# Performance work log

Measured on AMD Instinct MI355X. Metric: run time of the kernel, lower is better.

The kernel has to match this reference:

```python
import jax, jax.numpy as jnp
import numpy as np

NODES_PER_GRAPH = 116
HEADS = 2
D_HEAD = 116  # out_channels per head
HID = 256
B = 512
N = B * NODES_PER_GRAPH
DEG = 8
E = N * DEG
D_OUT = HEADS * D_HEAD  # 232


def setup_inputs() -> dict:
    key = jax.random.key(0)
    ks = jax.random.split(key, 6)
    h_flat = jax.random.normal(ks[0], (N, HID), dtype=jnp.float32)
    # every node receives DEG edges from random nodes within its own 116-node graph
    dst = jnp.repeat(jnp.arange(N, dtype=jnp.int64), DEG)
    offs = jax.random.randint(ks[1], (E,), 0, NODES_PER_GRAPH, dtype=jnp.int64)
    src = (dst // NODES_PER_GRAPH) * NODES_PER_GRAPH + offs
    edge_index = jnp.stack([src, dst], axis=0)
    batch_index = jnp.repeat(jnp.arange(B, dtype=jnp.int64), NODES_PER_GRAPH)
    s = 1.0 / np.sqrt(HID)
    Wq = jax.random.normal(ks[2], (HID, D_OUT), dtype=jnp.float32) * s
    Wk = jax.random.normal(ks[3], (HID, D_OUT), dtype=jnp.float32) * s
    Wv = jax.random.normal(ks[4], (HID, D_OUT), dtype=jnp.float32) * s
    Ws = jax.random.normal(ks[5], (HID, D_OUT), dtype=jnp.float32) * s
    return {"h_flat": h_flat, "edge_index": edge_index, "batch_index": batch_index,
            "Wq": Wq, "Wk": Wk, "Wv": Wv, "Ws": Ws}


def _graph_transformer_layer(h, edge_index, Wq, Wk, Wv, Ws):
    # PyG TransformerConv-style multi-head edge attention, concat heads + root skip.
    n = h.shape[0]
    q = (h @ Wq).reshape(n, HEADS, D_HEAD)
    k = (h @ Wk).reshape(n, HEADS, D_HEAD)
    v = (h @ Wv).reshape(n, HEADS, D_HEAD)
    src, dst = edge_index[0], edge_index[1]
    # per-edge scores [E, H]
    scores = jnp.einsum('ehd,ehd->eh', q[dst], k[src]) / np.sqrt(D_HEAD)
    # segment softmax over incoming edges of each dst node
    m = jax.ops.segment_max(scores, dst, num_segments=n)
    m = jnp.where(jnp.isfinite(m), m, 0.0)
    ex = jnp.exp(scores - m[dst])
    denom = jax.ops.segment_sum(ex, dst, num_segments=n)
    alpha_e = ex / (denom[dst] + 1e-16)
    msg = alpha_e[:, :, None] * v[src]                      # [E, H, Dh]
    attn = jax.ops.segment_sum(msg, dst, num_segments=n)    # [N, H, Dh]
    return attn.reshape(n, D_OUT) + h @ Ws


def reference(h_flat, edge_index, batch_index, Wq, Wk, Wv, Ws):
    n = h_flat.shape[0]
    b = n // NODES_PER_GRAPH
    h_proj = _graph_transformer_layer(h_flat, edge_index, Wq, Wk, Wv, Ws)  # [N, 232]
    e = h_proj.mean(axis=-1)                                 # [N]
    # scatter_softmax over per-graph node segments
    em = jax.ops.segment_max(e, batch_index, num_segments=b)
    ee = jnp.exp(e - em[batch_index])
    es = jax.ops.segment_sum(ee, batch_index, num_segments=b)
    alpha = ee / es[batch_index]                             # [N]
    h_weighted = alpha[:, None] * h_proj                     # [N, 232]
    alpha_map = alpha.reshape(b, NODES_PER_GRAPH)            # [B, 116]
    return alpha_map, h_weighted
```

## Files before the change

kernel.cpp:

```cpp
#include <hip/hip_runtime.h>

#define NODES  116
#define HEADS  2
#define DH     116
#define HID    256
#define NGRAPH 512
#define NN     (NGRAPH*NODES)
#define DEG    8
#define DOUT   (HEADS*DH)
#define NCOLS  928
#define NB_N   8
#define MB_N   464

typedef short  s8v  __attribute__((ext_vector_type(8)));
typedef float  f4v  __attribute__((ext_vector_type(4)));

static __device__ __forceinline__ float bf2f(unsigned short u) {
    union { unsigned int i; float f; } c; c.i = ((unsigned int)u) << 16; return c.f;
}
static __device__ __forceinline__ unsigned short f2bf(float f) {
    union { float f; unsigned int u; } c; c.f = f;
    unsigned int u = c.u;
    unsigned int r = (u + 0x7FFFu + ((u >> 16) & 1u)) >> 16;
    return (unsigned short)r;
}

#define GLD_LDS16(gptr, lptr) \
    __builtin_amdgcn_global_load_lds((const __attribute__((address_space(1))) void*)(gptr), \
                                     (__attribute__((address_space(3))) void*)(lptr), 16, 0, 0)

__global__ __launch_bounds__(256) void prep_h(const float* __restrict__ h,
                                              unsigned short* __restrict__ hs)
{
    unsigned int f = blockIdx.x * 256 + threadIdx.x;
    unsigned int m    = f & 127;
    unsigned int quad = (f >> 7) & 3;
    unsigned int kb   = (f >> 9) & 7;
    unsigned int Mb   = f >> 12;
    unsigned int row  = Mb * 128 + m;
    unsigned int k    = kb * 32 + quad * 8;
    const float4 v0 = *(const float4*)(h + (size_t)row * HID + k);
    const float4 v1 = *(const float4*)(h + (size_t)row * HID + k + 4);
    unsigned short o[8] = { f2bf(v0.x), f2bf(v0.y), f2bf(v0.z), f2bf(v0.w),
                            f2bf(v1.x), f2bf(v1.y), f2bf(v1.z), f2bf(v1.w) };
    *(uint4*)(hs + (size_t)f * 8) = *(const uint4*)o;
}

__global__ __launch_bounds__(256) void prep_w(const float* __restrict__ Wq,
                                              const float* __restrict__ Wk,
                                              const float* __restrict__ Wv,
                                              const float* __restrict__ Ws,
                                              unsigned short* __restrict__ wt)
{
    unsigned int f = blockIdx.x * 256 + threadIdx.x;
    unsigned int n    = f & 127;
    unsigned int quad = (f >> 7) & 3;
    unsigned int kb   = (f >> 9) & 7;
    unsigned int Nb   = f >> 12;
    unsigned int gcol = Nb * 128 + n;
    unsigned int k    = kb * 32 + quad * 8;
    unsigned short o[8] = {0,0,0,0,0,0,0,0};
    if (gcol < NCOLS) {
        unsigned int sel = gcol / DOUT;
        unsigned int col = gcol - sel * DOUT;
        const float* W = (sel == 0) ? Wq : (sel == 1) ? Wk : (sel == 2) ? Wv : Ws;
        #pragma unroll
        for (int i = 0; i < 8; i++)
            o[i] = f2bf(W[(size_t)(k + i) * DOUT + col]);
    }
    *(uint4*)(wt + (size_t)f * 8) = *(const uint4*)o;
}

__global__ __launch_bounds__(256) void gemm_mfma(const unsigned short* __restrict__ hs,
                                                 const unsigned short* __restrict__ wt,
                                                 unsigned short* __restrict__ qkvs)
{
    __shared__ unsigned short lds[17408];
    unsigned short* aA = lds;
    unsigned short* bB = lds + 4096;

    const int by  = blockIdx.x;
    const int bx  = blockIdx.y;
    const int tid = threadIdx.x;
    const int w    = tid >> 6;
    const int lane = tid & 63;
    const int wr   = w >> 1;
    const int wc   = w & 1;
    const int l15  = lane & 15;
    const int quad = lane >> 4;

    f4v acc[4][4];
    #pragma unroll
    for (int mt = 0; mt < 4; mt++)
        #pragma unroll
        for (int nt = 0; nt < 4; nt++)
            #pragma unroll
            for (int r = 0; r < 4; r++) acc[mt][nt][r] = 0.0f;

    for (int kb = 0; kb < 8; kb++) {
        const char* gA = (const char*)(hs + ((size_t)(bx * 8 + kb)) * 4096);
        const char* gB = (const char*)(wt + ((size_t)(by * 8 + kb)) * 4096);
        #pragma unroll
        for (int j = 0; j < 2; j++) {
            int c = w * 2 + j;
            GLD_LDS16(gA + (c * 64 + lane) * 16, (char*)aA + c * 1024);
            GLD_LDS16(gB + (c * 64 + lane) * 16, (char*)bB + c * 1024);
        }
        __syncthreads();

        s8v a[4], b[4];
        #pragma unroll
        for (int mt = 0; mt < 4; mt++) {
            int m = wr * 64 + mt * 16 + l15;
            a[mt] = *(const s8v*)(aA + (quad * 128 + m) * 8);
        }
        #pragma unroll
        for (int nt = 0; nt < 4; nt++) {
            int n = wc * 64 + nt * 16 + l15;
            b[nt] = *(const s8v*)(bB + (quad * 128 + n) * 8);
        }
        #pragma unroll
        for (int mt = 0; mt < 4; mt++)
            #pragma unroll
            for (int nt = 0; nt < 4; nt++)
                acc[mt][nt] = __builtin_amdgcn_mfma_f32_16x16x32_bf16(
                    a[mt], b[nt], acc[mt][nt], 0, 0, 0);
        __syncthreads();
    }

    unsigned short* cb = lds;
    #pragma unroll
    for (int mt = 0; mt < 4; mt++) {
        #pragma unroll
        for (int nt = 0; nt < 4; nt++) {
            int col = wc * 64 + nt * 16 + l15;
            #pragma unroll
            for (int r = 0; r < 4; r++) {
                int row = wr * 64 + mt * 16 + quad * 4 + r;
                cb[row * 136 + col] = f2bf(acc[mt][nt][r]);
            }
        }
    }
    __syncthreads();

    #pragma unroll
    for (int i = 0; i < 8; i++) {
        int g   = tid + i * 256;
        int row = g >> 4;
        int gi  = g & 15;
        int gcol = by * 128 + gi * 8;
        if (gcol < NCOLS) {
            const uint2 p0 = *(const uint2*)(cb + row * 136 + gi * 8);
            const uint2 p1 = *(const uint2*)(cb + row * 136 + gi * 8 + 4);
            uint4 p = make_uint4(p0.x, p0.y, p1.x, p1.y);
            *(uint4*)(qkvs + (size_t)(bx * 128 + row) * NCOLS + gcol) = p;
        }
    }
}

__global__ __launch_bounds__(1024) void attn_fused(const unsigned short* __restrict__ qkvs,
                                                   const int* __restrict__ eidx,
                                                   float* __restrict__ out_alpha,
                                                   float* __restrict__ out_hw)
{
    __shared__ unsigned short k_l[NODES * DOUT];
    __shared__ unsigned short v_l[NODES * DOUT];
    __shared__ int   srcl[NODES * DEG];
    __shared__ float part[NODES * 8];
    __shared__ float ew[NODES];
    __shared__ float alph[NODES];
    __shared__ float red[2];

    const int g   = blockIdx.x;
    const int tid = threadIdx.x;
    const unsigned short* base = qkvs + (size_t)g * NODES * NCOLS;

    for (int idx = tid; idx < NODES * DEG; idx += 1024)
        srcl[idx] = eidx[(size_t)g * NODES * DEG + idx] - g * NODES;
    for (int f = tid; f < NODES * 29; f += 1024) {
        int r  = f / 29;
        int gi = f - r * 29;
        *(uint4*)(k_l + r * DOUT + gi * 8) = *(const uint4*)(base + r * NCOLS + 232 + gi * 8);
        *(uint4*)(v_l + r * DOUT + gi * 8) = *(const uint4*)(base + r * NCOLS + 464 + gi * 8);
    }
    __syncthreads();

    const bool act = (tid < NODES * 8);
    const int i   = tid >> 3;
    const int seg = tid & 7;
    const int hd  = seg >> 2;
    const int s4  = seg & 3;
    const int dbase = hd * DH + s4 * 32;
    const int g4  = (s4 == 3) ? 5 : 8;

    int   sj[DEG];
    float av[DEG];
    float hp[32];

    if (act) {
        #pragma unroll
        for (int j = 0; j < DEG; j++) sj[j] = srcl[i * DEG + j];

        float s[DEG];
        #pragma unroll
        for (int j = 0; j < DEG; j++) s[j] = 0.0f;
        const unsigned short* qrow = base + i * NCOLS + dbase;
        #pragma unroll
        for (int gg = 0; gg < 8; gg++) {
            if (gg < g4) {
                uint2 qg = *(const uint2*)(qrow + gg * 4);
                float q0 = bf2f((unsigned short)(qg.x & 0xFFFF));
                float q1 = bf2f((unsigned short)(qg.x >> 16));
                float q2 = bf2f((unsigned short)(qg.y & 0xFFFF));
                float q3 = bf2f((unsigned short)(qg.y >> 16));
                #pragma unroll
                for (int j = 0; j < DEG; j++) {
                    uint2 kg = *(const uint2*)(k_l + sj[j] * DOUT + dbase + gg * 4);
                    s[j] += q0 * bf2f((unsigned short)(kg.x & 0xFFFF));
                    s[j] += q1 * bf2f((unsigned short)(kg.x >> 16));
                    s[j] += q2 * bf2f((unsigned short)(kg.y & 0xFFFF));
                    s[j] += q3 * bf2f((unsigned short)(kg.y >> 16));
                }
            }
        }
        #pragma unroll
        for (int j = 0; j < DEG; j++) {
            s[j] += __shfl_xor(s[j], 1);
            s[j] += __shfl_xor(s[j], 2);
        }
        const float scale = 0.09284766908852594f;
        float m = -1e30f;
        #pragma unroll
        for (int j = 0; j < DEG; j++) { s[j] *= scale; m = fmaxf(m, s[j]); }
        float ssum = 0.0f;
        #pragma unroll
        for (int j = 0; j < DEG; j++) { s[j] = __expf(s[j] - m); ssum += s[j]; }
        float inv = 1.0f / ssum;
        #pragma unroll
        for (int j = 0; j < DEG; j++) av[j] = s[j] * inv;

        const unsigned short* srow = base + i * NCOLS + 696 + dbase;
        #pragma unroll
        for (int gg = 0; gg < 8; gg++) {
            if (gg < g4) {
                uint2 sg = *(const uint2*)(srow + gg * 4);
                hp[gg*4+0] = bf2f((unsigned short)(sg.x & 0xFFFF));
                hp[gg*4+1] = bf2f((unsigned short)(sg.x >> 16));
                hp[gg*4+2] = bf2f((unsigned short)(sg.y & 0xFFFF));
                hp[gg*4+3] = bf2f((unsigned short)(sg.y >> 16));
            } else {
                hp[gg*4+0] = 0.f; hp[gg*4+1] = 0.f; hp[gg*4+2] = 0.f; hp[gg*4+3] = 0.f;
            }
        }
        #pragma unroll
        for (int j = 0; j < DEG; j++) {
            float a = av[j];
            const unsigned short* vrow = v_l + sj[j] * DOUT + dbase;
            #pragma unroll
            for (int gg = 0; gg < 8; gg++) {
                if (gg < g4) {
                    uint2 vg = *(const uint2*)(vrow + gg * 4);
                    hp[gg*4+0] += a * bf2f((unsigned short)(vg.x & 0xFFFF));
                    hp[gg*4+1] += a * bf2f((unsigned short)(vg.x >> 16));
                    hp[gg*4+2] += a * bf2f((unsigned short)(vg.y & 0xFFFF));
                    hp[gg*4+3] += a * bf2f((unsigned short)(vg.y >> 16));
                }
            }
        }
        float rs = 0.0f;
        #pragma unroll
        for (int d = 0; d < 32; d++) rs += hp[d];
        part[tid] = rs;
    }
    __syncthreads();

    if (tid < NODES) {
        float e = 0.0f;
        #pragma unroll
        for (int j = 0; j < 8; j++) e += part[tid * 8 + j];
        ew[tid] = e * (1.0f / DOUT);
    }
    __syncthreads();
    if (tid < 64) {
        float a = ew[tid];
        float b = (tid + 64 < NODES) ? ew[tid + 64] : -1e30f;
        float mm = fmaxf(a, b);
        #pragma unroll
        for (int off = 32; off > 0; off >>= 1) mm = fmaxf(mm, __shfl_down(mm, off));
        if (tid == 0) red[0] = mm;
    }
    __syncthreads();
    if (tid < NODES) ew[tid] = __expf(ew[tid] - red[0]);
    __syncthreads();
    if (tid < 64) {
        float a = ew[tid] + ((tid + 64 < NODES) ? ew[tid + 64] : 0.0f);
        #pragma unroll
        for (int off = 32; off > 0; off >>= 1) a += __shfl_down(a, off);
        if (tid == 0) red[1] = a;
    }
    __syncthreads();
    if (tid < NODES) {
        float al = ew[tid] / red[1];
        alph[tid] = al;
        out_alpha[(size_t)g * NODES + tid] = al;
    }
    __syncthreads();

    if (act) {
        float al = alph[i];
        float* orow = out_hw + (size_t)(g * NODES + i) * DOUT + dbase;
        #pragma unroll
        for (int gg = 0; gg < 8; gg++) {
            if (gg < g4) {
                float4 o = make_float4(al * hp[gg*4+0], al * hp[gg*4+1],
                                       al * hp[gg*4+2], al * hp[gg*4+3]);
                *(float4*)(orow + gg * 4) = o;
            }
        }
    }
}

extern "C" void kernel_launch(void* const* d_in, const int* in_sizes, int n_in,
                              void* d_out, int out_size, void* d_ws, size_t ws_size,
                              hipStream_t stream)
{
    const float* h    = (const float*)d_in[0];
    const int*   eidx = (const int*)d_in[1];
    const float* Wq   = (const float*)d_in[3];
    const float* Wk   = (const float*)d_in[4];
    const float* Wv   = (const float*)d_in[5];
    const float* Ws   = (const float*)d_in[6];

    unsigned short* qkvs = (unsigned short*)d_ws;
    unsigned short* hs   = qkvs + (size_t)NN * NCOLS;
    unsigned short* wt   = hs + (size_t)NN * HID;

    float* out_alpha = (float*)d_out;
    float* out_hw    = out_alpha + NN;

    prep_h<<<7424, 256, 0, stream>>>(h, hs);
    prep_w<<<128, 256, 0, stream>>>(Wq, Wk, Wv, Ws, wt);
    gemm_mfma<<<dim3(NB_N, MB_N), 256, 0, stream>>>(hs, wt, qkvs);
    attn_fused<<<NGRAPH, 1024, 0, stream>>>(qkvs, eidx, out_alpha, out_hw);
}
```

Baseline: 249.2 us.

## Fuse per-graph QKVS GEMM with edge attention, split heads across blocks

The standalone GEMM that wrote the full Q/K/V/S projection to global memory is replaced by a per-graph, per-head fused kernel. Each block computes that graph's 116x116 Q, K, V and skip tiles with MFMA into LDS, using double-buffered async global-to-LDS loads. It then runs edge attention in LDS and writes only the head output plus row sums. A small second kernel does the per-graph softmax pooling. This removes the large intermediate global round trip, at the cost of padding rows and columns from 116 to 128 (wasted MFMA work), heavy LDS use that limits occupancy, and a bf16 intermediate for h_proj.

After: 238.9 us. -4.1%, faster.

```diff
diff --git a/kernel.cpp b/kernel.cpp
--- a/kernel.cpp
+++ b/kernel.cpp
@@ -8,9 +8,7 @@
 #define NN     (NGRAPH*NODES)
 #define DEG    8
 #define DOUT   (HEADS*DH)
-#define NCOLS  928
-#define NB_N   8
-#define MB_N   464
+#define RSTR   120
 
 typedef short  s8v  __attribute__((ext_vector_type(8)));
 typedef float  f4v  __attribute__((ext_vector_type(4)));
@@ -36,13 +34,16 @@
     unsigned int m    = f & 127;
     unsigned int quad = (f >> 7) & 3;
     unsigned int kb   = (f >> 9) & 7;
-    unsigned int Mb   = f >> 12;
-    unsigned int row  = Mb * 128 + m;
-    unsigned int k    = kb * 32 + quad * 8;
-    const float4 v0 = *(const float4*)(h + (size_t)row * HID + k);
-    const float4 v1 = *(const float4*)(h + (size_t)row * HID + k + 4);
-    unsigned short o[8] = { f2bf(v0.x), f2bf(v0.y), f2bf(v0.z), f2bf(v0.w),
-                            f2bf(v1.x), f2bf(v1.y), f2bf(v1.z), f2bf(v1.w) };
+    unsigned int g    = f >> 12;
+    unsigned short o[8] = {0,0,0,0,0,0,0,0};
+    if (m < NODES) {
+        unsigned int row = g * NODES + m;
+        unsigned int k   = kb * 32 + quad * 8;
+        const float4 v0 = *(const float4*)(h + (size_t)row * HID + k);
+        const float4 v1 = *(const float4*)(h + (size_t)row * HID + k + 4);
+        o[0]=f2bf(v0.x); o[1]=f2bf(v0.y); o[2]=f2bf(v0.z); o[3]=f2bf(v0.w);
+        o[4]=f2bf(v1.x); o[5]=f2bf(v1.y); o[6]=f2bf(v1.z); o[7]=f2bf(v1.w);
+    }
     *(uint4*)(hs + (size_t)f * 8) = *(const uint4*)o;
 }
 
@@ -56,14 +57,13 @@
     unsigned int n    = f & 127;
     unsigned int quad = (f >> 7) & 3;
     unsigned int kb   = (f >> 9) & 7;
-    unsigned int Nb   = f >> 12;
-    unsigned int gcol = Nb * 128 + n;
-    unsigned int k    = kb * 32 + quad * 8;
+    unsigned int ch   = (f >> 12) & 3;
+    unsigned int hd   = f >> 14;
     unsigned short o[8] = {0,0,0,0,0,0,0,0};
-    if (gcol < NCOLS) {
-        unsigned int sel = gcol / DOUT;
-        unsigned int col = gcol - sel * DOUT;
-        const float* W = (sel == 0) ? Wq : (sel == 1) ? Wk : (sel == 2) ? Wv : Ws;
+    if (n < NODES) {
+        unsigned int col = hd * DH + n;
+        unsigned int k   = kb * 32 + quad * 8;
+        const float* W = (ch == 0) ? Wq : (ch == 1) ? Wk : (ch == 2) ? Wv : Ws;
         #pragma unroll
         for (int i = 0; i < 8; i++)
             o[i] = f2bf(W[(size_t)(k + i) * DOUT + col]);
@@ -71,215 +71,169 @@
     *(uint4*)(wt + (size_t)f * 8) = *(const uint4*)o;
 }
 
-__global__ __launch_bounds__(256) void gemm_mfma(const unsigned short* __restrict__ hs,
+__global__ __launch_bounds__(1024) void fused_k1(const unsigned short* __restrict__ hs,
                                                  const unsigned short* __restrict__ wt,
-                                                 unsigned short* __restrict__ qkvs)
-{
-    __shared__ unsigned short lds[17408];
-    unsigned short* aA = lds;
-    unsigned short* bB = lds + 4096;
-
-    const int by  = blockIdx.x;
-    const int bx  = blockIdx.y;
+                                                 const int* __restrict__ eidx,
+                                                 unsigned short* __restrict__ hp,
+                                                 float* __restrict__ psums)
+{
+    __shared__ unsigned short stA[2][4096];
+    __shared__ unsigned short stB[2][4096];
+    __shared__ unsigned short ql[NODES * RSTR];
+    __shared__ unsigned short kl[NODES * RSTR];
+    __shared__ unsigned short vl[NODES * RSTR];
+    __shared__ unsigned short sl[NODES * RSTR];
+    __shared__ int   srcl[NODES * DEG];
+    __shared__ float alph[NODES * DEG];
+
+    const int b   = blockIdx.x;
+    const int g   = b & 511;
+    const int hd  = b >> 9;
     const int tid = threadIdx.x;
     const int w    = tid >> 6;
     const int lane = tid & 63;
-    const int wr   = w >> 1;
-    const int wc   = w & 1;
     const int l15  = lane & 15;
     const int quad = lane >> 4;
-
-    f4v acc[4][4];
+    const int wm   = w >> 2;
+    const int wn   = w & 3;
+
+    if (tid < NODES * DEG)
+        srcl[tid] = eidx[(size_t)g * NODES * DEG + tid] - g * NODES;
+
+    const char* gA = (const char*)(hs + (size_t)g * 32768);
+    const char* gB = (const char*)(wt + (size_t)hd * 4 * 8 * 4096);
+
+    #define ISSUE(s, buf) do {                                                   \
+        int _kb = (s) & 7, _ch = (s) >> 3;                                       \
+        if (w < 8) { GLD_LDS16(gA + _kb * 8192 + w * 1024 + lane * 16,           \
+                               (char*)stA[buf] + w * 1024); }                    \
+        else       { int _w8 = w - 8;                                            \
+                     GLD_LDS16(gB + (_ch * 8 + _kb) * 8192 + _w8 * 1024 + lane * 16, \
+                               (char*)stB[buf] + _w8 * 1024); }                  \
+    } while (0)
+
+    f4v acc[2][2];
     #pragma unroll
-    for (int mt = 0; mt < 4; mt++)
-        #pragma unroll
-        for (int nt = 0; nt < 4; nt++)
-            #pragma unroll
-            for (int r = 0; r < 4; r++) acc[mt][nt][r] = 0.0f;
-
-    for (int kb = 0; kb < 8; kb++) {
-        const char* gA = (const char*)(hs + ((size_t)(bx * 8 + kb)) * 4096);
-        const char* gB = (const char*)(wt + ((size_t)(by * 8 + kb)) * 4096);
-        #pragma unroll
-        for (int j = 0; j < 2; j++) {
-            int c = w * 2 + j;
-            GLD_LDS16(gA + (c * 64 + lane) * 16, (char*)aA + c * 1024);
-            GLD_LDS16(gB + (c * 64 + lane) * 16, (char*)bB + c * 1024);
-        }
+    for (int i = 0; i < 2; i++)
+        #pragma unroll
+        for (int j = 0; j < 2; j++)
+            #pragma unroll
+            for (int r = 0; r < 4; r++) acc[i][j][r] = 0.0f;
+
+    ISSUE(0, 0);
+    for (int s = 0; s < 32; s++) {
         __syncthreads();
-
-        s8v a[4], b[4];
-        #pragma unroll
-        for (int mt = 0; mt < 4; mt++) {
-            int m = wr * 64 + mt * 16 + l15;
-            a[mt] = *(const s8v*)(aA + (quad * 128 + m) * 8);
-        }
-        #pragma unroll
-        for (int nt = 0; nt < 4; nt++) {
-            int n = wc * 64 + nt * 16 + l15;
-            b[nt] = *(const s8v*)(bB + (quad * 128 + n) * 8);
-        }
-        #pragma unroll
-        for (int mt = 0; mt < 4; mt++)
-            #pragma unroll
-            for (int nt = 0; nt < 4; nt++)
-                acc[mt][nt] = __builtin_amdgcn_mfma_f32_16x16x32_bf16(
-                    a[mt], b[nt], acc[mt][nt], 0, 0, 0);
-        __syncthreads();
-    }
-
-    unsigned short* cb = lds;
-    #pragma unroll
-    for (int mt = 0; mt < 4; mt++) {
-        #pragma unroll
-        for (int nt = 0; nt < 4; nt++) {
-            int col = wc * 64 + nt * 16 + l15;
-            #pragma unroll
-            for (int r = 0; r < 4; r++) {
-                int row = wr * 64 + mt * 16 + quad * 4 + r;
-                cb[row * 136 + col] = f2bf(acc[mt][nt][r]);
+        if (s < 31) ISSUE(s + 1, (s + 1) & 1);
+        const unsigned short* A = stA[s & 1];
+        const unsigned short* B = stB[s & 1];
+        s8v a[2], bb[2];
+        #pragma unroll
+        for (int t = 0; t < 2; t++) {
+            int m = wm * 32 + t * 16 + l15;
+            a[t]  = *(const s8v*)(A + (quad * 128 + m) * 8);
+            int n = wn * 32 + t * 16 + l15;
+            bb[t] = *(const s8v*)(B + (quad * 128 + n) * 8);
+        }
+        #pragma unroll
+        for (int i = 0; i < 2; i++)
+            #pragma unroll
+            for (int j = 0; j < 2; j++)
+                acc[i][j] = __builtin_amdgcn_mfma_f32_16x16x32_bf16(a[i], bb[j], acc[i][j], 0, 0, 0);
+
+        if ((s & 7) == 7) {
+            int ch = s >> 3;
+            unsigned short* dst = (ch == 0) ? ql : (ch == 1) ? kl : (ch == 2) ? vl : sl;
+            #pragma unroll
+            for (int i = 0; i < 2; i++) {
+                #pragma unroll
+                for (int j = 0; j < 2; j++) {
+                    int col = wn * 32 + j * 16 + l15;
+                    #pragma unroll
+                    for (int r = 0; r < 4; r++) {
+                        int row = wm * 32 + i * 16 + quad * 4 + r;
+                        if (row < NODES && col < NODES)
+                            dst[row * RSTR + col] = f2bf(acc[i][j][r]);
+                        acc[i][j][r] = 0.0f;
+                    }
+                }
             }
         }
     }
     __syncthreads();
 
-    #pragma unroll
-    for (int i = 0; i < 8; i++) {
-        int g   = tid + i * 256;
-        int row = g >> 4;
-        int gi  = g & 15;
-        int gcol = by * 128 + gi * 8;
-        if (gcol < NCOLS) {
-            const uint2 p0 = *(const uint2*)(cb + row * 136 + gi * 8);
-            const uint2 p1 = *(const uint2*)(cb + row * 136 + gi * 8 + 4);
-            uint4 p = make_uint4(p0.x, p0.y, p1.x, p1.y);
-            *(uint4*)(qkvs + (size_t)(bx * 128 + row) * NCOLS + gcol) = p;
-        }
-    }
-}
-
-__global__ __launch_bounds__(1024) void attn_fused(const unsigned short* __restrict__ qkvs,
-                                                   const int* __restrict__ eidx,
-                                                   float* __restrict__ out_alpha,
-                                                   float* __restrict__ out_hw)
-{
-    __shared__ unsigned short k_l[NODES * DOUT];
-    __shared__ unsigned short v_l[NODES * DOUT];
-    __shared__ int   srcl[NODES * DEG];
-    __shared__ float part[NODES * 8];
+    if (tid < NODES * DEG) {
+        const int i = tid >> 3;
+        const int src = srcl[tid];
+        float s = 0.0f;
+        #pragma unroll 4
+        for (int gi = 0; gi < 29; gi++) {
+            uint2 qg = *(const uint2*)(ql + i * RSTR + gi * 4);
+            uint2 kg = *(const uint2*)(kl + src * RSTR + gi * 4);
+            s += bf2f((unsigned short)(qg.x & 0xFFFF)) * bf2f((unsigned short)(kg.x & 0xFFFF));
+            s += bf2f((unsigned short)(qg.x >> 16))    * bf2f((unsigned short)(kg.x >> 16));
+            s += bf2f((unsigned short)(qg.y & 0xFFFF)) * bf2f((unsigned short)(kg.y & 0xFFFF));
+            s += bf2f((unsigned short)(qg.y >> 16))    * bf2f((unsigned short)(kg.y >> 16));
+        }
+        s *= 0.09284766908852594f;
+        float m = s;
+        m = fmaxf(m, __shfl_xor(m, 1));
+        m = fmaxf(m, __shfl_xor(m, 2));
+        m = fmaxf(m, __shfl_xor(m, 4));
+        float e = __expf(s - m);
+        float sum = e;
+        sum += __shfl_xor(sum, 1);
+        sum += __shfl_xor(sum, 2);
+        sum += __shfl_xor(sum, 4);
+        alph[tid] = e / sum;
+    }
+    __syncthreads();
+
+    if (tid < NODES * DEG) {
+        const int i  = tid >> 3;
+        const int cs = tid & 7;
+        float al[DEG]; int sj[DEG];
+        #pragma unroll
+        for (int j = 0; j < DEG; j++) { al[j] = alph[i * DEG + j]; sj[j] = srcl[i * DEG + j]; }
+        float rsum = 0.0f;
+        for (int c = cs; c < NODES; c += 8) {
+            float v = bf2f(sl[i * RSTR + c]);
+            #pragma unroll
+            for (int j = 0; j < DEG; j++)
+                v += al[j] * bf2f(vl[sj[j] * RSTR + c]);
+            ql[i * RSTR + c] = f2bf(v);
+            rsum += v;
+        }
+        rsum += __shfl_xor(rsum, 1);
+        rsum += __shfl_xor(rsum, 2);
+        rsum += __shfl_xor(rsum, 4);
+        if (cs == 0) psums[((size_t)hd * NGRAPH + g) * NODES + i] = rsum;
+    }
+    __syncthreads();
+
+    for (int f = tid; f < NODES * 29; f += 1024) {
+        int r  = f / 29;
+        int gi = f - r * 29;
+        *(uint2*)(hp + ((size_t)(g * NODES + r)) * DOUT + hd * DH + gi * 4) =
+            *(const uint2*)(ql + r * RSTR + gi * 4);
+    }
+    #undef ISSUE
+}
+
+__global__ __launch_bounds__(256) void pool_k2(const unsigned short* __restrict__ hp,
+                                               const float* __restrict__ psums,
+                                               float* __restrict__ out_alpha,
+                                               float* __restrict__ out_hw)
+{
     __shared__ float ew[NODES];
     __shared__ float alph[NODES];
     __shared__ float red[2];
 
     const int g   = blockIdx.x;
     const int tid = threadIdx.x;
-    const unsigned short* base = qkvs + (size_t)g * NODES * NCOLS;
-
-    for (int idx = tid; idx < NODES * DEG; idx += 1024)
-        srcl[idx] = eidx[(size_t)g * NODES * DEG + idx] - g * NODES;
-    for (int f = tid; f < NODES * 29; f += 1024) {
-        int r  = f / 29;
-        int gi = f - r * 29;
-        *(uint4*)(k_l + r * DOUT + gi * 8) = *(const uint4*)(base + r * NCOLS + 232 + gi * 8);
-        *(uint4*)(v_l + r * DOUT + gi * 8) = *(const uint4*)(base + r * NCOLS + 464 + gi * 8);
-    }
-    __syncthreads();
-
-    const bool act = (tid < NODES * 8);
-    const int i   = tid >> 3;
-    const int seg = tid & 7;
-    const int hd  = seg >> 2;
-    const int s4  = seg & 3;
-    const int dbase = hd * DH + s4 * 32;
-    const int g4  = (s4 == 3) ? 5 : 8;
-
-    int   sj[DEG];
-    float av[DEG];
-    float hp[32];
-
-    if (act) {
-        #pragma unroll
-        for (int j = 0; j < DEG; j++) sj[j] = srcl[i * DEG + j];
-
-        float s[DEG];
-        #pragma unroll
-        for (int j = 0; j < DEG; j++) s[j] = 0.0f;
-        const unsigned short* qrow = base + i * NCOLS + dbase;
-        #pragma unroll
-        for (int gg = 0; gg < 8; gg++) {
-            if (gg < g4) {
-                uint2 qg = *(const uint2*)(qrow + gg * 4);
-                float q0 = bf2f((unsigned short)(qg.x & 0xFFFF));
-                float q1 = bf2f((unsigned short)(qg.x >> 16));
-                float q2 = bf2f((unsigned short)(qg.y & 0xFFFF));
-                float q3 = bf2f((unsigned short)(qg.y >> 16));
-                #pragma unroll
-                for (int j = 0; j < DEG; j++) {
-                    uint2 kg = *(const uint2*)(k_l + sj[j] * DOUT + dbase + gg * 4);
-                    s[j] += q0 * bf2f((unsigned short)(kg.x & 0xFFFF));
-                    s[j] += q1 * bf2f((unsigned short)(kg.x >> 16));
-                    s[j] += q2 * bf2f((unsigned short)(kg.y & 0xFFFF));
-                    s[j] += q3 * bf2f((unsigned short)(kg.y >> 16));
-                }
-            }
-        }
-        #pragma unroll
-        for (int j = 0; j < DEG; j++) {
-            s[j] += __shfl_xor(s[j], 1);
-            s[j] += __shfl_xor(s[j], 2);
-        }
-        const float scale = 0.09284766908852594f;
-        float m = -1e30f;
-        #pragma unroll
-        for (int j = 0; j < DEG; j++) { s[j] *= scale; m = fmaxf(m, s[j]); }
-        float ssum = 0.0f;
-        #pragma unroll
-        for (int j = 0; j < DEG; j++) { s[j] = __expf(s[j] - m); ssum += s[j]; }
-        float inv = 1.0f / ssum;
-        #pragma unroll
-        for (int j = 0; j < DEG; j++) av[j] = s[j] * inv;
-
-        const unsigned short* srow = base + i * NCOLS + 696 + dbase;
-        #pragma unroll
-        for (int gg = 0; gg < 8; gg++) {
-            if (gg < g4) {
-                uint2 sg = *(const uint2*)(srow + gg * 4);
-                hp[gg*4+0] = bf2f((unsigned short)(sg.x & 0xFFFF));
-                hp[gg*4+1] = bf2f((unsigned short)(sg.x >> 16));
-                hp[gg*4+2] = bf2f((unsigned short)(sg.y & 0xFFFF));
-                hp[gg*4+3] = bf2f((unsigned short)(sg.y >> 16));
-            } else {
-                hp[gg*4+0] = 0.f; hp[gg*4+1] = 0.f; hp[gg*4+2] = 0.f; hp[gg*4+3] = 0.f;
-            }
-        }
-        #pragma unroll
-        for (int j = 0; j < DEG; j++) {
-            float a = av[j];
-            const unsigned short* vrow = v_l + sj[j] * DOUT + dbase;
-            #pragma unroll
-            for (int gg = 0; gg < 8; gg++) {
-                if (gg < g4) {
-                    uint2 vg = *(const uint2*)(vrow + gg * 4);
-                    hp[gg*4+0] += a * bf2f((unsigned short)(vg.x & 0xFFFF));
-                    hp[gg*4+1] += a * bf2f((unsigned short)(vg.x >> 16));
-                    hp[gg*4+2] += a * bf2f((unsigned short)(vg.y & 0xFFFF));
-                    hp[gg*4+3] += a * bf2f((unsigned short)(vg.y >> 16));
-                }
-            }
-        }
-        float rs = 0.0f;
-        #pragma unroll
-        for (int d = 0; d < 32; d++) rs += hp[d];
-        part[tid] = rs;
-    }
-    __syncthreads();
-
-    if (tid < NODES) {
-        float e = 0.0f;
-        #pragma unroll
-        for (int j = 0; j < 8; j++) e += part[tid * 8 + j];
-        ew[tid] = e * (1.0f / DOUT);
-    }
+
+    if (tid < NODES)
+        ew[tid] = (psums[(size_t)g * NODES + tid] +
+                   psums[((size_t)NGRAPH + g) * NODES + tid]) * (1.0f / DOUT);
     __syncthreads();
     if (tid < 64) {
         float a = ew[tid];
@@ -306,17 +260,16 @@
     }
     __syncthreads();
 
-    if (act) {
-        float al = alph[i];
-        float* orow = out_hw + (size_t)(g * NODES + i) * DOUT + dbase;
-        #pragma unroll
-        for (int gg = 0; gg < 8; gg++) {
-            if (gg < g4) {
-                float4 o = make_float4(al * hp[gg*4+0], al * hp[gg*4+1],
-                                       al * hp[gg*4+2], al * hp[gg*4+3]);
-                *(float4*)(orow + gg * 4) = o;
-            }
-        }
+    for (int f = tid; f < NODES * 58; f += 256) {
+        int r  = f / 58;
+        int gi = f - r * 58;
+        float al = alph[r];
+        uint2 hv = *(const uint2*)(hp + ((size_t)(g * NODES + r)) * DOUT + gi * 4);
+        float4 o = make_float4(al * bf2f((unsigned short)(hv.x & 0xFFFF)),
+                               al * bf2f((unsigned short)(hv.x >> 16)),
+                               al * bf2f((unsigned short)(hv.y & 0xFFFF)),
+                               al * bf2f((unsigned short)(hv.y >> 16)));
+        *(float4*)(out_hw + ((size_t)(g * NODES + r)) * DOUT + gi * 4) = o;
     }
 }
 
@@ -331,15 +284,16 @@
     const float* Wv   = (const float*)d_in[5];
     const float* Ws   = (const float*)d_in[6];
 
-    unsigned short* qkvs = (unsigned short*)d_ws;
-    unsigned short* hs   = qkvs + (size_t)NN * NCOLS;
-    unsigned short* wt   = hs + (size_t)NN * HID;
+    unsigned short* hs = (unsigned short*)d_ws;
+    unsigned short* wt = hs + (size_t)16777216;
+    unsigned short* hp = wt + (size_t)262144;
+    float*       psums = (float*)(hp + (size_t)13778944);
 
     float* out_alpha = (float*)d_out;
     float* out_hw    = out_alpha + NN;
 
-    prep_h<<<7424, 256, 0, stream>>>(h, hs);
+    prep_h<<<8192, 256, 0, stream>>>(h, hs);
     prep_w<<<128, 256, 0, stream>>>(Wq, Wk, Wv, Ws, wt);
-    gemm_mfma<<<dim3(NB_N, MB_N), 256, 0, stream>>>(hs, wt, qkvs);
-    attn_fused<<<NGRAPH, 1024, 0, stream>>>(qkvs, eidx, out_alpha, out_hw);
-}
+    fused_k1<<<1024, 1024, 0, stream>>>(hs, wt, eidx, hp, psums);
+    pool_k2<<<NGRAPH, 256, 0, stream>>>(hp, psums, out_alpha, out_hw);
+}
```
